# Optimization experiments

Measured on AMD Instinct MI355X. Metric: run time of the kernel, lower is better.

## Reference

```python
import jax, jax.numpy as jnp
import numpy as np

B, T, WIN, CIN, H, COUT = 512, 64, 256, 4, 512, 2


def setup_inputs() -> dict:
    key = jax.random.key(0)
    k = jax.random.split(key, 4)
    D = WIN * CIN  # 1024
    s = 0.02
    return {
        "inputs": jax.random.normal(k[0], (B, T, WIN, CIN), dtype=jnp.float32),
        "W_in": jax.random.normal(k[1], (D, 3 * H), dtype=jnp.float32) * s,
        "b_in": jnp.zeros((3 * H,), dtype=jnp.float32),
        "U": jax.random.normal(k[2], (H, 3 * H), dtype=jnp.float32) * s,
        "b_rec": jnp.zeros((3 * H,), dtype=jnp.float32),
        "W2": jax.random.normal(k[3], (2 * H, WIN * COUT), dtype=jnp.float32) * s,
        "b2": jnp.zeros((WIN * COUT,), dtype=jnp.float32),
    }


def _gru_last_state(x, W_in, b_in, U, b_rec):
    # Keras GRU v2 math: reset_after=True, recurrent_activation=sigmoid,
    # activation=relu (as configured). training=False -> no dropout.
    Bm, Tm, _ = x.shape
    Hm = U.shape[0]
    # precompute input projections for all timesteps: [B, T, 3H]
    xg = jnp.einsum("btd,dh->bth", x, W_in) + b_in

    def step(h, xg_t):
        hg = h @ U + b_rec  # recurrent bias applied before reset gate (reset_after)
        xz, xr, xh = jnp.split(xg_t, 3, axis=-1)
        hz, hr, hh = jnp.split(hg, 3, axis=-1)
        z = jax.nn.sigmoid(xz + hz)
        r = jax.nn.sigmoid(xr + hr)
        h_cand = jax.nn.relu(xh + r * hh)
        h_new = z * h + (1.0 - z) * h_cand
        return h_new, None

    h0 = jnp.zeros((Bm, Hm), dtype=x.dtype)
    hT, _ = jax.lax.scan(step, h0, jnp.swapaxes(xg, 0, 1))
    return hT  # [B, H]; with return_sequences=False, output == final_state


def reference(inputs, W_in, b_in, U, b_rec, W2, b2):
    Bm, Tm = inputs.shape[0], inputs.shape[1]
    x = inputs.reshape(Bm, Tm, -1)  # flatten window*channels -> [B, T, 1024]
    hT = _gru_last_state(x, W_in, b_in, U, b_rec)
    cat = jnp.concatenate([hT, hT], axis=-1)  # tf.concat((output, final_state))
    out = cat @ W2 + b2
    return out.reshape(Bm, WIN, COUT)
```

## Files before the change

### kernel.cpp

```cpp
#include <hip/hip_runtime.h>
#include <hip/hip_bf16.h>
#include <stdint.h>

#define BATCH 512
#define TSTEPS 64
#define DIN 1024
#define HID 512
#define G3 1536
#define MROWS (BATCH * TSTEPS)
#define POUT 512

typedef __attribute__((ext_vector_type(8))) short bf16x8;
typedef __attribute__((ext_vector_type(4))) float f32x4;

__device__ __forceinline__ float bf2f(short s) {
  union { unsigned u; float f; } v;
  v.u = ((unsigned)(unsigned short)s) << 16;
  return v.f;
}
__device__ __forceinline__ short f2bf(float f) {
  __hip_bfloat16 h = __float2bfloat16(f);
  short s;
  __builtin_memcpy(&s, &h, 2);
  return s;
}
__device__ __forceinline__ void gload_lds16(const void* g, void* l) {
  __builtin_amdgcn_global_load_lds(
      (const __attribute__((address_space(1))) void*)g,
      (__attribute__((address_space(3))) void*)l, 16, 0, 0);
}

__global__ __launch_bounds__(256) void transpose_cast(const float* __restrict__ in,
                                                      short* __restrict__ out,
                                                      int R, int C) {
  __shared__ float tile[32][33];
  const int c0 = blockIdx.x * 32, r0 = blockIdx.y * 32;
  const int tx = threadIdx.x & 31, ty = threadIdx.x >> 5;
#pragma unroll
  for (int i = 0; i < 4; ++i) {
    const int r = r0 + ty + i * 8;
    tile[ty + i * 8][tx] = in[(size_t)r * C + c0 + tx];
  }
  __syncthreads();
#pragma unroll
  for (int i = 0; i < 4; ++i) {
    const int c = c0 + ty + i * 8;
    out[(size_t)c * R + r0 + tx] = f2bf(tile[tx][ty + i * 8]);
  }
}

__global__ __launch_bounds__(256) void u_pack2(const float* __restrict__ U,
                                               short* __restrict__ Upk2) {
  const unsigned idx = blockIdx.x * 256 + threadIdx.x;
  const unsigned e = idx & 7u;
  unsigned tmp = idx >> 3;
  const unsigned lc = tmp & 15u; tmp >>= 4;
  const unsigned lg = tmp & 3u;  tmp >>= 2;
  const unsigned wn = tmp & 3u;  tmp >>= 2;
  const unsigned f = tmp % 48u;
  const unsigned cg = tmp / 48u;
  const unsigned g = f >> 4, kc = f & 15u;
  const unsigned k = kc * 32u + lg * 8u + e;
  const unsigned col = g * 512u + cg * 64u + wn * 16u + lc;
  Upk2[idx] = f2bf(U[(size_t)k * G3 + col]);
}

__global__ __launch_bounds__(256) void gemm_xg_mfma(const float* __restrict__ X,
                                                    const short* __restrict__ Wt,
                                                    const float* __restrict__ bin,
                                                    __hip_bfloat16* __restrict__ XG) {
  __shared__ __align__(16) short As[128 * 64];
  __shared__ __align__(16) short Bs[128 * 64];
  const int tid = threadIdx.x;
  const int w = tid >> 6, l = tid & 63;
  const int lc = l & 15, lg = l >> 4;

  const int xcd = blockIdx.x & 7;
  const int idx = blockIdx.x >> 3;
  const int wg = xcd * 384 + idx;
  const int rt = wg / 12, ct = wg % 12;
  const int row0 = rt * 128, col0 = ct * 128;

  const int wm = w >> 1, wn = w & 1;

  f32x4 acc[4][4];
#pragma unroll
  for (int mt = 0; mt < 4; ++mt)
#pragma unroll
    for (int nt = 0; nt < 4; ++nt) acc[mt][nt] = (f32x4){0.f, 0.f, 0.f, 0.f};

  const int tr = tid >> 3, p = tid & 7;

  for (int k0 = 0; k0 < DIN; k0 += 64) {
    float4 ar[4][2];
#pragma unroll
    for (int i = 0; i < 4; ++i) {
      const int r = i * 32 + tr;
      const int s = p ^ (r & 7);
      const float* xp = &X[(size_t)(row0 + r) * DIN + k0 + s * 8];
      ar[i][0] = *reinterpret_cast<const float4*>(xp);
      ar[i][1] = *reinterpret_cast<const float4*>(xp + 4);
    }
    __syncthreads();
#pragma unroll
    for (int i = 0; i < 4; ++i) {
      const int r = i * 32 + tr;
      bf16x8 v;
      v[0] = f2bf(ar[i][0].x); v[1] = f2bf(ar[i][0].y);
      v[2] = f2bf(ar[i][0].z); v[3] = f2bf(ar[i][0].w);
      v[4] = f2bf(ar[i][1].x); v[5] = f2bf(ar[i][1].y);
      v[6] = f2bf(ar[i][1].z); v[7] = f2bf(ar[i][1].w);
      *reinterpret_cast<bf16x8*>((char*)As + r * 128 + p * 16) = v;
    }
#pragma unroll
    for (int i = 0; i < 4; ++i) {
      const int rr = w * 32 + i * 8 + (l >> 3);
      const int pp = l & 7;
      const int s = pp ^ (rr & 7);
      gload_lds16(&Wt[(size_t)(col0 + rr) * DIN + k0 + s * 8],
                  (char*)Bs + (w * 32 + i * 8) * 128);
    }
    __syncthreads();
#pragma unroll
    for (int kc = 0; kc < 2; ++kc) {
      bf16x8 a[4], b[4];
#pragma unroll
      for (int mt = 0; mt < 4; ++mt) {
        const int R = wm * 64 + mt * 16 + lc;
        const int ch = (kc * 4 + lg) ^ (R & 7);
        a[mt] = *reinterpret_cast<const bf16x8*>((const char*)As + R * 128 + ch * 16);
      }
#pragma unroll
      for (int nt = 0; nt < 4; ++nt) {
        const int Rn = wn * 64 + nt * 16 + lc;
        const int ch = (kc * 4 + lg) ^ (Rn & 7);
        b[nt] = *reinterpret_cast<const bf16x8*>((const char*)Bs + Rn * 128 + ch * 16);
      }
#pragma unroll
      for (int mt = 0; mt < 4; ++mt)
#pragma unroll
        for (int nt = 0; nt < 4; ++nt)
          acc[mt][nt] = __builtin_amdgcn_mfma_f32_16x16x32_bf16(a[mt], b[nt],
                                                                acc[mt][nt], 0, 0, 0);
    }
  }

  float bv[4];
#pragma unroll
  for (int nt = 0; nt < 4; ++nt) bv[nt] = bin[col0 + wn * 64 + nt * 16 + lc];
#pragma unroll
  for (int mt = 0; mt < 4; ++mt) {
#pragma unroll
    for (int nt = 0; nt < 4; ++nt) {
      const int col = col0 + wn * 64 + nt * 16 + lc;
      const int g = col >> 9;
      const int rem = col & 511;
      const int cgc = rem >> 6, cc = rem & 63;
#pragma unroll
      for (int rr = 0; rr < 4; ++rr) {
        const int m = row0 + wm * 64 + mt * 16 + lg * 4 + rr;
        const int t = m & 63, b = m >> 6;
        const size_t o =
            ((((size_t)t * 16 + (b >> 5)) * 8 + cgc) * 32 + (b & 31)) * 192 +
            g * 64 + cc;
        XG[o] = __float2bfloat16(acc[mt][nt][rr] + bv[nt]);
      }
    }
  }
}

__global__ __launch_bounds__(512, 2) void gru_scan_coop(
    const __hip_bfloat16* __restrict__ XG, const short* __restrict__ Upk2,
    const float* __restrict__ brec, short* h_g, unsigned* bar,
    float* __restrict__ HT) {
  __shared__ __align__(16) short hS[32 * 512];
  __shared__ __align__(16) short xgL[2][6144];
  const int tid = threadIdx.x, w = tid >> 6, l = tid & 63;
  const int lc = l & 15, lg = l >> 4;
  const int bg = blockIdx.x >> 3, cgi = blockIdx.x & 7;
  const int b0 = bg * 32, c0 = cgi * 64;
  const int wm = w & 1, wn = w >> 1;
  unsigned* const flags = bar + bg * 16;

  bf16x8 ub[3][16];
#pragma unroll
  for (int g = 0; g < 3; ++g)
#pragma unroll
    for (int kc = 0; kc < 16; ++kc)
      ub[g][kc] = *reinterpret_cast<const bf16x8*>(
          Upk2 + ((((size_t)cgi * 48 + g * 16 + kc) * 4 + wn) * 4 + lg) * 128 +
          lc * 8);

  for (int i = tid; i < 4096; i += 512) ((unsigned long long*)hS)[i] = 0ull;

  const short* XGs = (const short*)XG;
  {
    const short* xs = XGs + ((size_t)bg * 8 + cgi) * 6144;
    gload_lds16(xs + tid * 8, (char*)xgL[0] + w * 1024);
    if (tid < 256)
      gload_lds16(xs + (512 + tid) * 8, (char*)xgL[0] + 8192 + w * 1024);
  }

  const int j = c0 + wn * 16 + lc;
  const float brz = brec[j], brr = brec[512 + j], brh = brec[1024 + j];
  const int arow = wm * 16 + lc;

  __syncthreads();

  for (int t = 0; t < TSTEPS; ++t) {
    f32x4 za0 = (f32x4){0.f, 0.f, 0.f, 0.f}, za1 = za0, za2 = za0;
    if (t > 0) {
      for (;;) {
        const unsigned f = __hip_atomic_load(&flags[l & 7], __ATOMIC_RELAXED,
                                             __HIP_MEMORY_SCOPE_AGENT);
        if (__all((int)(f >= (unsigned)t))) break;
        __builtin_amdgcn_s_sleep(1);
      }
      const unsigned long long* hsrc = (const unsigned long long*)(
          h_g + ((size_t)(t & 1) * BATCH + b0) * 512);
      unsigned long long v[8];
#pragma unroll
      for (int r = 0; r < 8; ++r)
        v[r] = __hip_atomic_load(hsrc + r * 512 + tid, __ATOMIC_RELAXED,
                                 __HIP_MEMORY_SCOPE_AGENT);
#pragma unroll
      for (int r = 0; r < 8; ++r)
        ((unsigned long long*)hS)[r * 512 + tid] = v[r];
      __syncthreads();

#pragma unroll
      for (int kc = 0; kc < 16; ++kc) {
        const int s = kc * 4 + lg;
        const bf16x8 a = *(const bf16x8*)((const char*)hS + arow * 1024 +
                                          ((s ^ (arow & 7)) << 4));
        za0 = __builtin_amdgcn_mfma_f32_16x16x32_bf16(a, ub[0][kc], za0, 0, 0, 0);
        za1 = __builtin_amdgcn_mfma_f32_16x16x32_bf16(a, ub[1][kc], za1, 0, 0, 0);
        za2 = __builtin_amdgcn_mfma_f32_16x16x32_bf16(a, ub[2][kc], za2, 0, 0, 0);
      }
    }

    const short* xb = xgL[t & 1];
#pragma unroll
    for (int r = 0; r < 4; ++r) {
      const int lb = wm * 16 + lg * 4 + r;
      const float xz = bf2f(xb[lb * 192 + wn * 16 + lc]);
      const float xr = bf2f(xb[lb * 192 + 64 + wn * 16 + lc]);
      const float xh = bf2f(xb[lb * 192 + 128 + wn * 16 + lc]);
      const float z = 1.f / (1.f + __expf(-(xz + za0[r] + brz)));
      const float rg = 1.f / (1.f + __expf(-(xr + za1[r] + brr)));
      const float hc = fmaxf(fmaf(rg, za2[r] + brh, xh), 0.f);
      const int hoff = lb * 1024 + (((j >> 3) ^ (lb & 7)) << 4) + (j & 7) * 2;
      const float hold = bf2f(*(const short*)((const char*)hS + hoff));
      const float hnew = fmaf(z, hold - hc, hc);
      if (t == TSTEPS - 1) {
        HT[(size_t)(b0 + lb) * HID + j] = hnew;
      } else {
        __hip_atomic_store(
            (unsigned short*)((char*)h_g +
                              ((size_t)((t + 1) & 1) * BATCH + b0) * 1024 + hoff),
            (unsigned short)f2bf(hnew), __ATOMIC_RELAXED,
            __HIP_MEMORY_SCOPE_AGENT);
      }
    }
    if (t == TSTEPS - 1) break;

    __syncthreads();
    if (tid == 0)
      __hip_atomic_store(&flags[cgi], (unsigned)(t + 1), __ATOMIC_RELAXED,
                         __HIP_MEMORY_SCOPE_AGENT);
    {
      const short* xs = XGs + (((size_t)(t + 1) * 16 + bg) * 8 + cgi) * 6144;
      char* xd = (char*)xgL[(t + 1) & 1];
      gload_lds16(xs + tid * 8, xd + w * 1024);
      if (tid < 256)
        gload_lds16(xs + (512 + tid) * 8, xd + 8192 + w * 1024);
    }
  }
}

__global__ __launch_bounds__(256) void final_proj(const float* __restrict__ HT,
                                                  const float* __restrict__ W2,
                                                  const float* __restrict__ b2,
                                                  float* __restrict__ OUT) {
  const int b = blockIdx.x >> 1;
  const int pp = ((blockIdx.x & 1) << 8) + threadIdx.x;
  float acc = b2[pp];
  const float* h = &HT[(size_t)b * HID];
  for (int k = 0; k < HID; ++k)
    acc = fmaf(h[k], W2[(size_t)k * POUT + pp] + W2[(size_t)(k + HID) * POUT + pp], acc);
  OUT[(size_t)b * POUT + pp] = acc;
}

extern "C" void kernel_launch(void* const* d_in, const int* in_sizes, int n_in,
                              void* d_out, int out_size, void* d_ws,
                              size_t ws_size, hipStream_t stream) {
  const float* X    = (const float*)d_in[0];
  const float* Win  = (const float*)d_in[1];
  const float* bin  = (const float*)d_in[2];
  const float* U    = (const float*)d_in[3];
  const float* brec = (const float*)d_in[4];
  const float* W2   = (const float*)d_in[5];
  const float* b2   = (const float*)d_in[6];
  float* OUT = (float*)d_out;

  char* ws = (char*)d_ws;
  size_t off = 0;
  __hip_bfloat16* XG = (__hip_bfloat16*)(ws + off); off += (size_t)MROWS * G3 * 2;
  short* Wt   = (short*)(ws + off); off += (size_t)G3 * DIN * 2;
  short* Upk2 = (short*)(ws + off); off += (size_t)G3 * HID * 2;
  float* HT   = (float*)(ws + off); off += (size_t)BATCH * HID * 4;
  short* h_g  = (short*)(ws + off); off += (size_t)2 * BATCH * HID * 2;
  unsigned* bar = (unsigned*)(ws + off);

  hipMemsetAsync(bar, 0, 1024, stream);

  transpose_cast<<<dim3(G3 / 32, DIN / 32), 256, 0, stream>>>(Win, Wt, DIN, G3);
  u_pack2<<<(HID * G3) / 256, 256, 0, stream>>>(U, Upk2);
  gemm_xg_mfma<<<(MROWS / 128) * (G3 / 128), 256, 0, stream>>>(X, Wt, bin, XG);

  const __hip_bfloat16* XGc = XG;
  const short* Upkc = Upk2;
  void* args[] = {(void*)&XGc, (void*)&Upkc, (void*)&brec,
                  (void*)&h_g, (void*)&bar, (void*)&HT};
  hipLaunchCooperativeKernel((const void*)gru_scan_coop, dim3(128), dim3(512),
                             args, 0, stream);

  final_proj<<<(BATCH * POUT) / 256, 256, 0, stream>>>(HT, W2, b2, OUT);
}
```

Before: 470.6 us.

## Fuse input-projection GEMM with GRU scan to overlap per-timestep production

Merges the input-projection GEMM and the cooperative GRU scan into one launch. The first 128 blocks run the scan and the remaining blocks compute timestep-ordered GEMM tiles, bumping a per-timestep done counter that the scan spins on before prefetching that step's gate inputs. This lets the serial recurrence start while later timesteps' projections are still being computed, hiding most of the GEMM time. It drops the cooperative launch and assumes the scan blocks are resident alongside GEMM blocks, which risks deadlock if they are not scheduled first. The XG layout is also changed to a transposed per-gate form so stores can be packed 64-bit.

Measured after the change: 724.6 us. 54.0% more time.

```diff
diff --git a/kernel.cpp b/kernel.cpp
--- a/kernel.cpp
+++ b/kernel.cpp
@@ -9,6 +9,8 @@
 #define G3 1536
 #define MROWS (BATCH * TSTEPS)
 #define POUT 512
+#define NSCAN 128
+#define NGEMM 3072
 
 typedef __attribute__((ext_vector_type(8))) short bf16x8;
 typedef __attribute__((ext_vector_type(4))) float f32x4;
@@ -65,118 +67,124 @@
   Upk2[idx] = f2bf(U[(size_t)k * G3 + col]);
 }
 
-__global__ __launch_bounds__(256) void gemm_xg_mfma(const float* __restrict__ X,
-                                                    const short* __restrict__ Wt,
-                                                    const float* __restrict__ bin,
-                                                    __hip_bfloat16* __restrict__ XG) {
-  __shared__ __align__(16) short As[128 * 64];
-  __shared__ __align__(16) short Bs[128 * 64];
+__global__ __launch_bounds__(512, 2) void fused_gemm_scan(
+    const float* __restrict__ X, const short* __restrict__ Wt,
+    const float* __restrict__ bin, __hip_bfloat16* __restrict__ XG,
+    const short* __restrict__ Upk2, const float* __restrict__ brec,
+    short* h_g, unsigned* bar, float* __restrict__ HT) {
+  __shared__ __align__(16) char smem[57344];
   const int tid = threadIdx.x;
   const int w = tid >> 6, l = tid & 63;
   const int lc = l & 15, lg = l >> 4;
-
-  const int xcd = blockIdx.x & 7;
-  const int idx = blockIdx.x >> 3;
-  const int wg = xcd * 384 + idx;
-  const int rt = wg / 12, ct = wg % 12;
-  const int row0 = rt * 128, col0 = ct * 128;
-
-  const int wm = w >> 1, wn = w & 1;
-
-  f32x4 acc[4][4];
-#pragma unroll
-  for (int mt = 0; mt < 4; ++mt)
-#pragma unroll
-    for (int nt = 0; nt < 4; ++nt) acc[mt][nt] = (f32x4){0.f, 0.f, 0.f, 0.f};
-
-  const int tr = tid >> 3, p = tid & 7;
-
-  for (int k0 = 0; k0 < DIN; k0 += 64) {
-    float4 ar[4][2];
-#pragma unroll
-    for (int i = 0; i < 4; ++i) {
-      const int r = i * 32 + tr;
-      const int s = p ^ (r & 7);
-      const float* xp = &X[(size_t)(row0 + r) * DIN + k0 + s * 8];
-      ar[i][0] = *reinterpret_cast<const float4*>(xp);
-      ar[i][1] = *reinterpret_cast<const float4*>(xp + 4);
+  unsigned* const done = bar + 256;
+
+  if (blockIdx.x >= NSCAN) {
+    short* As = (short*)smem;
+    short* Bs = (short*)(smem + 16384);
+    const int bid2 = blockIdx.x - NSCAN;
+    const int xcd = bid2 & 7;
+    const int idx = bid2 >> 3;
+    const int gslot = idx / 12, ct = idx % 12;
+    const int g = gslot * 8 + xcd;
+    const int t = g >> 2, bgrp = g & 3;
+    const int col0 = ct * 128;
+    const int wm = w >> 2, wn = w & 3;
+
+    f32x4 acc[4][2];
+#pragma unroll
+    for (int mt = 0; mt < 4; ++mt)
+#pragma unroll
+      for (int nt = 0; nt < 2; ++nt) acc[mt][nt] = (f32x4){0.f, 0.f, 0.f, 0.f};
+
+    for (int k0 = 0; k0 < DIN; k0 += 64) {
+      float4 ar[2][2];
+      int arow_s[2], achk[2];
+#pragma unroll
+      for (int sl = 0; sl < 2; ++sl) {
+        const int s = sl * 512 + tid;
+        const int row = s >> 3, c = s & 7;
+        const int sc = c ^ (row & 7);
+        arow_s[sl] = row; achk[sl] = c;
+        const float* xp =
+            X + ((size_t)((bgrp * 128 + row) * 64 + t)) * DIN + k0 + sc * 8;
+        ar[sl][0] = *reinterpret_cast<const float4*>(xp);
+        ar[sl][1] = *reinterpret_cast<const float4*>(xp + 4);
+      }
+      __syncthreads();
+#pragma unroll
+      for (int sl = 0; sl < 2; ++sl) {
+        bf16x8 v;
+        v[0] = f2bf(ar[sl][0].x); v[1] = f2bf(ar[sl][0].y);
+        v[2] = f2bf(ar[sl][0].z); v[3] = f2bf(ar[sl][0].w);
+        v[4] = f2bf(ar[sl][1].x); v[5] = f2bf(ar[sl][1].y);
+        v[6] = f2bf(ar[sl][1].z); v[7] = f2bf(ar[sl][1].w);
+        *reinterpret_cast<bf16x8*>(As + arow_s[sl] * 64 + achk[sl] * 8) = v;
+      }
+#pragma unroll
+      for (int i = 0; i < 2; ++i) {
+        const int rr = w * 16 + i * 8 + (l >> 3);
+        const int pp = l & 7;
+        const int sc = pp ^ (rr & 7);
+        gload_lds16(&Wt[(size_t)(col0 + rr) * DIN + k0 + sc * 8],
+                    (char*)Bs + (w * 16 + i * 8) * 128);
+      }
+      __syncthreads();
+#pragma unroll
+      for (int kc = 0; kc < 2; ++kc) {
+        bf16x8 a[4], b[2];
+#pragma unroll
+        for (int mt = 0; mt < 4; ++mt) {
+          const int R = wm * 64 + mt * 16 + lc;
+          const int ch = (kc * 4 + lg) ^ (R & 7);
+          a[mt] = *reinterpret_cast<const bf16x8*>((const char*)As + R * 128 +
+                                                   ch * 16);
+        }
+#pragma unroll
+        for (int nt = 0; nt < 2; ++nt) {
+          const int Rn = wn * 32 + nt * 16 + lc;
+          const int ch = (kc * 4 + lg) ^ (Rn & 7);
+          b[nt] = *reinterpret_cast<const bf16x8*>((const char*)Bs + Rn * 128 +
+                                                   ch * 16);
+        }
+#pragma unroll
+        for (int mt = 0; mt < 4; ++mt)
+#pragma unroll
+          for (int nt = 0; nt < 2; ++nt)
+            acc[mt][nt] = __builtin_amdgcn_mfma_f32_16x16x32_bf16(
+                a[mt], b[nt], acc[mt][nt], 0, 0, 0);
+      }
+    }
+
+    unsigned long long* const XG64 = (unsigned long long*)XG;
+#pragma unroll
+    for (int mt = 0; mt < 4; ++mt) {
+#pragma unroll
+      for (int nt = 0; nt < 2; ++nt) {
+        const int col = col0 + wn * 32 + nt * 16 + lc;
+        const int gg = col >> 9, cg = (col >> 6) & 7, cc = col & 63;
+        const float bv = bin[col];
+        const int b_base = bgrp * 128 + wm * 64 + mt * 16 + lg * 4;
+        const int bg = b_base >> 5, bl = b_base & 31;
+        unsigned long long pk = 0;
+#pragma unroll
+        for (int rr = 0; rr < 4; ++rr)
+          pk |= (unsigned long long)(unsigned short)f2bf(acc[mt][nt][rr] + bv)
+                << (16 * rr);
+        const size_t offs = (((size_t)t * 16 + bg) * 8 + cg) * 6144 +
+                            gg * 2048 + cc * 32 + bl;
+        __hip_atomic_store(XG64 + (offs >> 2), pk, __ATOMIC_RELAXED,
+                           __HIP_MEMORY_SCOPE_AGENT);
+      }
     }
     __syncthreads();
-#pragma unroll
-    for (int i = 0; i < 4; ++i) {
-      const int r = i * 32 + tr;
-      bf16x8 v;
-      v[0] = f2bf(ar[i][0].x); v[1] = f2bf(ar[i][0].y);
-      v[2] = f2bf(ar[i][0].z); v[3] = f2bf(ar[i][0].w);
-      v[4] = f2bf(ar[i][1].x); v[5] = f2bf(ar[i][1].y);
-      v[6] = f2bf(ar[i][1].z); v[7] = f2bf(ar[i][1].w);
-      *reinterpret_cast<bf16x8*>((char*)As + r * 128 + p * 16) = v;
-    }
-#pragma unroll
-    for (int i = 0; i < 4; ++i) {
-      const int rr = w * 32 + i * 8 + (l >> 3);
-      const int pp = l & 7;
-      const int s = pp ^ (rr & 7);
-      gload_lds16(&Wt[(size_t)(col0 + rr) * DIN + k0 + s * 8],
-                  (char*)Bs + (w * 32 + i * 8) * 128);
-    }
-    __syncthreads();
-#pragma unroll
-    for (int kc = 0; kc < 2; ++kc) {
-      bf16x8 a[4], b[4];
-#pragma unroll
-      for (int mt = 0; mt < 4; ++mt) {
-        const int R = wm * 64 + mt * 16 + lc;
-        const int ch = (kc * 4 + lg) ^ (R & 7);
-        a[mt] = *reinterpret_cast<const bf16x8*>((const char*)As + R * 128 + ch * 16);
-      }
-#pragma unroll
-      for (int nt = 0; nt < 4; ++nt) {
-        const int Rn = wn * 64 + nt * 16 + lc;
-        const int ch = (kc * 4 + lg) ^ (Rn & 7);
-        b[nt] = *reinterpret_cast<const bf16x8*>((const char*)Bs + Rn * 128 + ch * 16);
-      }
-#pragma unroll
-      for (int mt = 0; mt < 4; ++mt)
-#pragma unroll
-        for (int nt = 0; nt < 4; ++nt)
-          acc[mt][nt] = __builtin_amdgcn_mfma_f32_16x16x32_bf16(a[mt], b[nt],
-                                                                acc[mt][nt], 0, 0, 0);
-    }
-  }
-
-  float bv[4];
-#pragma unroll
-  for (int nt = 0; nt < 4; ++nt) bv[nt] = bin[col0 + wn * 64 + nt * 16 + lc];
-#pragma unroll
-  for (int mt = 0; mt < 4; ++mt) {
-#pragma unroll
-    for (int nt = 0; nt < 4; ++nt) {
-      const int col = col0 + wn * 64 + nt * 16 + lc;
-      const int g = col >> 9;
-      const int rem = col & 511;
-      const int cgc = rem >> 6, cc = rem & 63;
-#pragma unroll
-      for (int rr = 0; rr < 4; ++rr) {
-        const int m = row0 + wm * 64 + mt * 16 + lg * 4 + rr;
-        const int t = m & 63, b = m >> 6;
-        const size_t o =
-            ((((size_t)t * 16 + (b >> 5)) * 8 + cgc) * 32 + (b & 31)) * 192 +
-            g * 64 + cc;
-        XG[o] = __float2bfloat16(acc[mt][nt][rr] + bv[nt]);
-      }
-    }
-  }
-}
-
-__global__ __launch_bounds__(512, 2) void gru_scan_coop(
-    const __hip_bfloat16* __restrict__ XG, const short* __restrict__ Upk2,
-    const float* __restrict__ brec, short* h_g, unsigned* bar,
-    float* __restrict__ HT) {
-  __shared__ __align__(16) short hS[32 * 512];
-  __shared__ __align__(16) short xgL[2][6144];
-  const int tid = threadIdx.x, w = tid >> 6, l = tid & 63;
-  const int lc = l & 15, lg = l >> 4;
+    if (tid == 0)
+      __hip_atomic_fetch_add(&done[t], 1u, __ATOMIC_RELAXED,
+                             __HIP_MEMORY_SCOPE_AGENT);
+    return;
+  }
+
+  short* hS = (short*)smem;
+  short* xgL = (short*)(smem + 32768);
   const int bg = blockIdx.x >> 3, cgi = blockIdx.x & 7;
   const int b0 = bg * 32, c0 = cgi * 64;
   const int wm = w & 1, wn = w >> 1;
@@ -194,11 +202,17 @@
   for (int i = tid; i < 4096; i += 512) ((unsigned long long*)hS)[i] = 0ull;
 
   const short* XGs = (const short*)XG;
+  if (tid == 0) {
+    while (__hip_atomic_load(&done[0], __ATOMIC_RELAXED,
+                             __HIP_MEMORY_SCOPE_AGENT) < 48u)
+      __builtin_amdgcn_s_sleep(1);
+  }
+  __syncthreads();
   {
     const short* xs = XGs + ((size_t)bg * 8 + cgi) * 6144;
-    gload_lds16(xs + tid * 8, (char*)xgL[0] + w * 1024);
+    gload_lds16(xs + tid * 8, (char*)xgL + w * 1024);
     if (tid < 256)
-      gload_lds16(xs + (512 + tid) * 8, (char*)xgL[0] + 8192 + w * 1024);
+      gload_lds16(xs + (512 + tid) * 8, (char*)xgL + 8192 + w * 1024);
   }
 
   const int j = c0 + wn * 16 + lc;
@@ -239,13 +253,14 @@
       }
     }
 
-    const short* xb = xgL[t & 1];
+    const short* xb = xgL + (t & 1) * 6144;
 #pragma unroll
     for (int r = 0; r < 4; ++r) {
       const int lb = wm * 16 + lg * 4 + r;
-      const float xz = bf2f(xb[lb * 192 + wn * 16 + lc]);
-      const float xr = bf2f(xb[lb * 192 + 64 + wn * 16 + lc]);
-      const float xh = bf2f(xb[lb * 192 + 128 + wn * 16 + lc]);
+      const int colloc = wn * 16 + lc;
+      const float xz = bf2f(xb[colloc * 32 + lb]);
+      const float xr = bf2f(xb[2048 + colloc * 32 + lb]);
+      const float xh = bf2f(xb[4096 + colloc * 32 + lb]);
       const float z = 1.f / (1.f + __expf(-(xz + za0[r] + brz)));
       const float rg = 1.f / (1.f + __expf(-(xr + za1[r] + brr)));
       const float hc = fmaxf(fmaf(rg, za2[r] + brh, xh), 0.f);
@@ -265,12 +280,17 @@
     if (t == TSTEPS - 1) break;
 
     __syncthreads();
-    if (tid == 0)
+    if (tid == 0) {
       __hip_atomic_store(&flags[cgi], (unsigned)(t + 1), __ATOMIC_RELAXED,
                          __HIP_MEMORY_SCOPE_AGENT);
+      while (__hip_atomic_load(&done[t + 1], __ATOMIC_RELAXED,
+                               __HIP_MEMORY_SCOPE_AGENT) < 48u)
+        __builtin_amdgcn_s_sleep(1);
+    }
+    __syncthreads();
     {
       const short* xs = XGs + (((size_t)(t + 1) * 16 + bg) * 8 + cgi) * 6144;
-      char* xd = (char*)xgL[(t + 1) & 1];
+      char* xd = (char*)xgL + ((t + 1) & 1) * 12288;
       gload_lds16(xs + tid * 8, xd + w * 1024);
       if (tid < 256)
         gload_lds16(xs + (512 + tid) * 8, xd + 8192 + w * 1024);
@@ -312,18 +332,13 @@
   short* h_g  = (short*)(ws + off); off += (size_t)2 * BATCH * HID * 2;
   unsigned* bar = (unsigned*)(ws + off);
 
-  hipMemsetAsync(bar, 0, 1024, stream);
+  hipMemsetAsync(bar, 0, 2048, stream);
 
   transpose_cast<<<dim3(G3 / 32, DIN / 32), 256, 0, stream>>>(Win, Wt, DIN, G3);
   u_pack2<<<(HID * G3) / 256, 256, 0, stream>>>(U, Upk2);
-  gemm_xg_mfma<<<(MROWS / 128) * (G3 / 128), 256, 0, stream>>>(X, Wt, bin, XG);
-
-  const __hip_bfloat16* XGc = XG;
-  const short* Upkc = Upk2;
-  void* args[] = {(void*)&XGc, (void*)&Upkc, (void*)&brec,
-                  (void*)&h_g, (void*)&bar, (void*)&HT};
-  hipLaunchCooperativeKernel((const void*)gru_scan_coop, dim3(128), dim3(512),
-                             args, 0, stream);
+
+  fused_gemm_scan<<<NSCAN + NGEMM, 512, 0, stream>>>(
+      X, Wt, bin, XG, Upk2, brec, h_g, bar, HT);
 
   final_proj<<<(BATCH * POUT) / 256, 256, 0, stream>>>(HT, W2, b2, OUT);
 }
```
